# Performance work log

Measured on AMD Instinct MI355X. Metric: run time of the kernel, lower is better.

The kernel has to match this reference:

```python
import jax, jax.numpy as jnp
import numpy as np

N = 50000   # nodes
E = 800000  # edges
F = 256     # in_channels
H = 256     # hidden (GCN output)


def setup_inputs() -> dict:
    key = jax.random.key(0)
    ks = jax.random.split(key, 6)
    x = jax.random.normal(ks[0], (N, F), jnp.float32)
    edge_index = jax.random.randint(ks[1], (2, E), 0, N)
    perm = jax.random.permutation(ks[2], N)
    W = jax.random.normal(ks[3], (F, H), jnp.float32) / np.sqrt(F)
    b = jnp.zeros((H,), jnp.float32)
    a = jnp.full((1,), 0.25, jnp.float32)  # PReLU slope
    disc_W = jax.random.normal(ks[4], (H, H), jnp.float32) / np.sqrt(H)
    return {"x": x, "W": W, "b": b, "a": a, "disc_W": disc_W,
            "edge_index": edge_index, "perm": perm}


def _gcn(x, W, b, src, dst, n):
    # GCNConv: linear -> symmetric-normalized aggregation (with self-loops) -> bias
    xw = x @ W  # [N, H]
    loop = jnp.arange(n)
    s = jnp.concatenate([src, loop])
    d = jnp.concatenate([dst, loop])
    ew = jnp.ones(s.shape[0], xw.dtype)
    deg = jax.ops.segment_sum(ew, d, num_segments=n)          # [N]
    dinv = jnp.where(deg > 0, jax.lax.rsqrt(deg), 0.0)
    norm = dinv[s] * dinv[d]                                   # [E+N]
    out = jax.ops.segment_sum(xw[s] * norm[:, None], d, num_segments=n)
    return out + b


def reference(x, W, b, a, disc_W, edge_index, perm):
    src, dst = edge_index[0], edge_index[1]
    n = x.shape[0]

    def encode(feat):
        h = _gcn(feat, W, b, src, dst, n)
        return jnp.where(h >= 0, h, a * h)  # PReLU

    z1 = encode(x)          # clean
    z2 = encode(x[perm])    # corrupted (row permutation)
    summary = jax.nn.sigmoid(z1.mean(axis=0))  # [H]
    wsum = disc_W @ summary                     # [H]
    pos = z1 @ wsum  # [N]
    neg = z2 @ wsum  # [N]
    return pos, neg
```

## Files before the change

kernel.cpp:

```cpp
#include <hip/hip_runtime.h>

#define N_NODES 50000
#define N_EDGES 800000
#define DIM 256
#define NB 196
#define UNROLL 8
#define MAXE (N_EDGES + N_NODES * UNROLL)
#define CSB 128
#define NCH 4
#define CCOLS 64
#define CHSZ (N_NODES * CCOLS)
#define RPB 16
#define CHB (N_NODES / RPB)

typedef __attribute__((ext_vector_type(8))) short bf16x8;
typedef __attribute__((ext_vector_type(4))) float f32x4;
typedef __attribute__((ext_vector_type(2))) float f32x2;

__device__ __forceinline__ unsigned int f2bf(float f) {
  unsigned int u = __float_as_uint(f);
  return (u + 0x7FFFu + ((u >> 16) & 1u)) >> 16;
}
__device__ __forceinline__ float bf_lo(unsigned int u) {
  return __uint_as_float(u << 16);
}
__device__ __forceinline__ float bf_hi(unsigned int u) {
  return __uint_as_float(u & 0xFFFF0000u);
}


__global__ void k_deg(const int* __restrict__ dst, int* __restrict__ deg) {
  int e = blockIdx.x * blockDim.x + threadIdx.x;
  if (e < N_EDGES) atomicAdd(&deg[dst[e]], 1);
}

__global__ __launch_bounds__(256) void k_alloc(const int* __restrict__ deg,
                                               float* __restrict__ dinv,
                                               int* __restrict__ gcur,
                                               int2* __restrict__ rse,
                                               int* __restrict__ cursor,
                                               uint2* __restrict__ meta) {
  __shared__ int s[256];
  __shared__ int base;
  const int t = threadIdx.x;
  const int i = blockIdx.x * 256 + t;
  int d = 0, pd = 0;
  if (i < N_NODES) {
    d = deg[i];
    dinv[i] = rsqrtf((float)(d + 1));
    pd = (d + UNROLL - 1) & ~(UNROLL - 1);
  }
  s[t] = pd;
  __syncthreads();
  for (int off = 1; off < 256; off <<= 1) {
    int u = (t >= off) ? s[t - off] : 0;
    __syncthreads();
    s[t] += u;
    __syncthreads();
  }
  if (t == 255) base = atomicAdd(gcur, s[255]);
  __syncthreads();
  if (i < N_NODES) {
    int rs = base + s[t] - pd;
    rse[i] = make_int2(rs, rs + pd);
    cursor[i] = rs;
    for (int j = d; j < pd; ++j) meta[rs + j] = make_uint2(0u, 0u);
  }
}

__global__ void k_scatter(const int* __restrict__ src, const int* __restrict__ dst,
                          const int* __restrict__ perm, const float* __restrict__ dinv,
                          int* __restrict__ cursor, uint2* __restrict__ meta) {
  int e = blockIdx.x * blockDim.x + threadIdx.x;
  if (e < N_EDGES) {
    int s = src[e], d = dst[e];
    int p = atomicAdd(&cursor[d], 1);
    meta[p] = make_uint2((unsigned)s | ((unsigned)perm[s] << 16),
                         __float_as_uint(dinv[s] * dinv[d]));
  }
}


__global__ void k_prep(const float* __restrict__ W, ushort* __restrict__ Wt) {
  int n = blockIdx.x, k = threadIdx.x;
  Wt[n * DIM + k] = (ushort)f2bf(W[k * DIM + n]);
}


__global__ __launch_bounds__(256) void k_gemm(const float* __restrict__ X,
                                              const ushort* __restrict__ Wt,
                                              ushort* __restrict__ XWC) {
  __shared__ ushort Xs[64 * 40];
  __shared__ ushort Ws[256 * 40];
  const int tid = threadIdx.x;
  const int lane = tid & 63;
  const int w = tid >> 6;
  const int m0 = blockIdx.x * 64;
  const int l16 = lane & 15, kh = lane >> 4;

  f32x4 acc[4][4];
#pragma unroll
  for (int mf = 0; mf < 4; ++mf)
#pragma unroll
    for (int nf = 0; nf < 4; ++nf) acc[mf][nf] = (f32x4){0.f, 0.f, 0.f, 0.f};

  for (int k0 = 0; k0 < DIM; k0 += 32) {
#pragma unroll
    for (int it = 0; it < 2; ++it) {
      int idx = tid + it * 256;
      int row = idx >> 3, q = idx & 7;
      int grow = m0 + row;
      float4 v = make_float4(0.f, 0.f, 0.f, 0.f);
      if (grow < N_NODES)
        v = *reinterpret_cast<const float4*>(&X[(size_t)grow * DIM + k0 + q * 4]);
      uint2 p;
      p.x = f2bf(v.x) | (f2bf(v.y) << 16);
      p.y = f2bf(v.z) | (f2bf(v.w) << 16);
      *reinterpret_cast<uint2*>(&Xs[row * 40 + q * 4]) = p;
    }
#pragma unroll
    for (int it = 0; it < 4; ++it) {
      int idx = tid + it * 256;
      int n = idx >> 2, c = idx & 3;
      uint4 wv = *reinterpret_cast<const uint4*>(&Wt[n * DIM + k0 + c * 8]);
      *reinterpret_cast<uint4*>(&Ws[n * 40 + c * 8]) = wv;
    }
    __syncthreads();
    bf16x8 a[4], b[4];
#pragma unroll
    for (int f = 0; f < 4; ++f) {
      a[f] = *reinterpret_cast<const bf16x8*>(&Ws[(w * 64 + f * 16 + l16) * 40 + kh * 8]);
      b[f] = *reinterpret_cast<const bf16x8*>(&Xs[(f * 16 + l16) * 40 + kh * 8]);
    }
#pragma unroll
    for (int mf = 0; mf < 4; ++mf)
#pragma unroll
      for (int nf = 0; nf < 4; ++nf)
        acc[mf][nf] = __builtin_amdgcn_mfma_f32_16x16x32_bf16(a[nf], b[mf],
                                                              acc[mf][nf], 0, 0, 0);
    __syncthreads();
  }
#pragma unroll
  for (int mf = 0; mf < 4; ++mf) {
    int m = m0 + mf * 16 + l16;
    if (m >= N_NODES) continue;
#pragma unroll
    for (int nf = 0; nf < 4; ++nf) {
      int cb = nf * 16 + kh * 4;
      uint2 p;
      p.x = f2bf(acc[mf][nf][0]) | (f2bf(acc[mf][nf][1]) << 16);
      p.y = f2bf(acc[mf][nf][2]) | (f2bf(acc[mf][nf][3]) << 16);
      *reinterpret_cast<uint2*>(&XWC[(size_t)w * CHSZ + (size_t)m * CCOLS + cb]) = p;
    }
  }
}


__device__ __forceinline__ void fma8v(f32x2* A, uint4 v, f32x2 n) {
  A[0] += (f32x2){__uint_as_float(v.x << 16), __uint_as_float(v.x)} * n;
  A[1] += (f32x2){__uint_as_float(v.y << 16), __uint_as_float(v.y)} * n;
  A[2] += (f32x2){__uint_as_float(v.z << 16), __uint_as_float(v.z)} * n;
  A[3] += (f32x2){__uint_as_float(v.w << 16), __uint_as_float(v.w)} * n;
}

__global__ __launch_bounds__(256) void k_aggc(
    const ushort* __restrict__ xwc, const int2* __restrict__ rse,
    const uint2* __restrict__ meta, const int* __restrict__ perm,
    const float* __restrict__ dinv, const float* __restrict__ bias,
    const float* __restrict__ slope, ushort* __restrict__ z1,
    ushort* __restrict__ z2) {
  const int blk = blockIdx.x;
  const int ch = blk / CHB;
  const int rb = blk % CHB;
  const int tid = threadIdx.x;
  const int r = rb * RPB + (tid >> 4);
  const int l = tid & 15;
  const int eg = l >> 3;
  const int sc = l & 7;
  const ushort* xc = xwc + (size_t)ch * CHSZ;
  const ushort* xcs = xc + sc * 8;
  const uint2* mp = meta + eg * 2;

  f32x2 a1[4] = {{0.f, 0.f}, {0.f, 0.f}, {0.f, 0.f}, {0.f, 0.f}};
  f32x2 a2[4] = {{0.f, 0.f}, {0.f, 0.f}, {0.f, 0.f}, {0.f, 0.f}};
  const int2 se = rse[r];
  int e = se.x;
  const int eEnd = se.y;
  if (e < eEnd) {
    uint4 m0 = *reinterpret_cast<const uint4*>(mp + e);
    uint4 m1 = *reinterpret_cast<const uint4*>(mp + e + 4);
    while (e < eEnd) {
      uint4 vA1 = *reinterpret_cast<const uint4*>(xcs + ((m0.x & 0xFFFFu) << 6));
      uint4 vA2 = *reinterpret_cast<const uint4*>(xcs + ((m0.x >> 16) << 6));
      uint4 vB1 = *reinterpret_cast<const uint4*>(xcs + ((m0.z & 0xFFFFu) << 6));
      uint4 vB2 = *reinterpret_cast<const uint4*>(xcs + ((m0.z >> 16) << 6));
      uint4 vC1 = *reinterpret_cast<const uint4*>(xcs + ((m1.x & 0xFFFFu) << 6));
      uint4 vC2 = *reinterpret_cast<const uint4*>(xcs + ((m1.x >> 16) << 6));
      uint4 vD1 = *reinterpret_cast<const uint4*>(xcs + ((m1.z & 0xFFFFu) << 6));
      uint4 vD2 = *reinterpret_cast<const uint4*>(xcs + ((m1.z >> 16) << 6));
      const int en = e + 8;
      const int ep = (en < eEnd) ? en : e;
      uint4 m0n = *reinterpret_cast<const uint4*>(mp + ep);
      uint4 m1n = *reinterpret_cast<const uint4*>(mp + ep + 4);
      const float fA = __uint_as_float(m0.y), fB = __uint_as_float(m0.w);
      const float fC = __uint_as_float(m1.y), fD = __uint_as_float(m1.w);
      const f32x2 nA = {fA, fA}, nB = {fB, fB}, nC = {fC, fC}, nD = {fD, fD};
      fma8v(a1, vA1, nA); fma8v(a2, vA2, nA);
      fma8v(a1, vB1, nB); fma8v(a2, vB2, nB);
      fma8v(a1, vC1, nC); fma8v(a2, vC2, nC);
      fma8v(a1, vD1, nD); fma8v(a2, vD2, nD);
      m0 = m0n; m1 = m1n;
      e = en;
    }
  }
#pragma unroll
  for (int j = 0; j < 4; ++j) {
    a1[j].x += __shfl_xor(a1[j].x, 8);
    a1[j].y += __shfl_xor(a1[j].y, 8);
    a2[j].x += __shfl_xor(a2[j].x, 8);
    a2[j].y += __shfl_xor(a2[j].y, 8);
  }
  if (eg == 0) {
    const float di = dinv[r];
    const float d2 = di * di;
    const f32x2 nd = {d2, d2};
    const int pr = perm[r];
    uint4 s1 = *reinterpret_cast<const uint4*>(xcs + ((unsigned)r << 6));
    uint4 s2 = *reinterpret_cast<const uint4*>(xcs + ((unsigned)pr << 6));
    fma8v(a1, s1, nd); fma8v(a2, s2, nd);
    const float* bp = bias + ch * CCOLS + sc * 8;
    float4 b0 = *reinterpret_cast<const float4*>(bp);
    float4 b1 = *reinterpret_cast<const float4*>(bp + 4);
    a1[0] += (f32x2){b0.x, b0.y}; a1[1] += (f32x2){b0.z, b0.w};
    a1[2] += (f32x2){b1.x, b1.y}; a1[3] += (f32x2){b1.z, b1.w};
    a2[0] += (f32x2){b0.x, b0.y}; a2[1] += (f32x2){b0.z, b0.w};
    a2[2] += (f32x2){b1.x, b1.y}; a2[3] += (f32x2){b1.z, b1.w};
    const float a0 = slope[0];
#pragma unroll
    for (int j = 0; j < 4; ++j) {
      a1[j].x = a1[j].x >= 0.f ? a1[j].x : a0 * a1[j].x;
      a1[j].y = a1[j].y >= 0.f ? a1[j].y : a0 * a1[j].y;
      a2[j].x = a2[j].x >= 0.f ? a2[j].x : a0 * a2[j].x;
      a2[j].y = a2[j].y >= 0.f ? a2[j].y : a0 * a2[j].y;
    }
    uint4 p1, p2;
    p1.x = f2bf(a1[0].x) | (f2bf(a1[0].y) << 16);
    p1.y = f2bf(a1[1].x) | (f2bf(a1[1].y) << 16);
    p1.z = f2bf(a1[2].x) | (f2bf(a1[2].y) << 16);
    p1.w = f2bf(a1[3].x) | (f2bf(a1[3].y) << 16);
    p2.x = f2bf(a2[0].x) | (f2bf(a2[0].y) << 16);
    p2.y = f2bf(a2[1].x) | (f2bf(a2[1].y) << 16);
    p2.z = f2bf(a2[2].x) | (f2bf(a2[2].y) << 16);
    p2.w = f2bf(a2[3].x) | (f2bf(a2[3].y) << 16);
    const size_t o = (size_t)r * DIM + ch * CCOLS + sc * 8;
    *reinterpret_cast<uint4*>(z1 + o) = p1;
    *reinterpret_cast<uint4*>(z2 + o) = p2;
  }
}


__global__ __launch_bounds__(256) void k_colsum(const ushort* __restrict__ z1,
                                                float* __restrict__ partial) {
  __shared__ float red[8 * 256];
  const int t = threadIdx.x;
  const int c8 = t & 31;
  const int g = t >> 5;
  float s[8] = {0.f, 0.f, 0.f, 0.f, 0.f, 0.f, 0.f, 0.f};
  for (int r = blockIdx.x * 8 + g; r < N_NODES; r += 8 * CSB) {
    uint4 v = *reinterpret_cast<const uint4*>(z1 + (size_t)r * DIM + c8 * 8);
    s[0] += bf_lo(v.x); s[1] += bf_hi(v.x);
    s[2] += bf_lo(v.y); s[3] += bf_hi(v.y);
    s[4] += bf_lo(v.z); s[5] += bf_hi(v.z);
    s[6] += bf_lo(v.w); s[7] += bf_hi(v.w);
  }
#pragma unroll
  for (int j = 0; j < 8; ++j) red[g * 256 + c8 * 8 + j] = s[j];
  __syncthreads();
  float tot = 0.f;
#pragma unroll
  for (int g2 = 0; g2 < 8; ++g2) tot += red[g2 * 256 + t];
  partial[blockIdx.x * 256 + t] = tot;
}

__global__ __launch_bounds__(256) void k_wsum(const float* __restrict__ partial,
                                              const float* __restrict__ disc_W,
                                              float* __restrict__ wsum) {
  __shared__ float s[DIM];
  const int t = threadIdx.x;
  float a0 = 0.f, a1 = 0.f, a2 = 0.f, a3 = 0.f;
  for (int b = 0; b < CSB; b += 4) {
    a0 += partial[(b + 0) * 256 + t];
    a1 += partial[(b + 1) * 256 + t];
    a2 += partial[(b + 2) * 256 + t];
    a3 += partial[(b + 3) * 256 + t];
  }
  float m = (a0 + a1 + a2 + a3) * (1.0f / (float)N_NODES);
  s[t] = 1.0f / (1.0f + expf(-m));
  __syncthreads();
  float acc = 0.f;
  for (int j = 0; j < DIM; j += 4) {
    float4 w4 = *reinterpret_cast<const float4*>(&disc_W[t * DIM + j]);
    acc += w4.x * s[j] + w4.y * s[j + 1] + w4.z * s[j + 2] + w4.w * s[j + 3];
  }
  wsum[t] = acc;
}


__global__ __launch_bounds__(256) void k_posneg(const ushort* __restrict__ z1,
                                                const ushort* __restrict__ z2,
                                                const float* __restrict__ wsum,
                                                float* __restrict__ pos,
                                                float* __restrict__ neg) {
  const int wid = (blockIdx.x * blockDim.x + threadIdx.x) >> 6;
  const int lane = threadIdx.x & 63;
  if (wid >= N_NODES) return;
  uint2 v1 = *reinterpret_cast<const uint2*>(z1 + (size_t)wid * DIM + lane * 4);
  uint2 v2 = *reinterpret_cast<const uint2*>(z2 + (size_t)wid * DIM + lane * 4);
  float4 w4 = *reinterpret_cast<const float4*>(&wsum[lane * 4]);
  float dp = bf_lo(v1.x) * w4.x + bf_hi(v1.x) * w4.y + bf_lo(v1.y) * w4.z + bf_hi(v1.y) * w4.w;
  float dn = bf_lo(v2.x) * w4.x + bf_hi(v2.x) * w4.y + bf_lo(v2.y) * w4.z + bf_hi(v2.y) * w4.w;
#pragma unroll
  for (int off = 32; off > 0; off >>= 1) {
    dp += __shfl_down(dp, off);
    dn += __shfl_down(dn, off);
  }
  if (lane == 0) { pos[wid] = dp; neg[wid] = dn; }
}


extern "C" void kernel_launch(void* const* d_in, const int* in_sizes, int n_in,
                              void* d_out, int out_size, void* d_ws, size_t ws_size,
                              hipStream_t stream) {
  const float* x      = (const float*)d_in[0];
  const float* W      = (const float*)d_in[1];
  const float* b      = (const float*)d_in[2];
  const float* a      = (const float*)d_in[3];
  const float* disc_W = (const float*)d_in[4];
  const int*   eidx   = (const int*)d_in[5];
  const int*   perm   = (const int*)d_in[6];
  const int* src = eidx;
  const int* dst = eidx + N_EDGES;

  constexpr size_t SZ_BFM  = (size_t)N_NODES * DIM * 2;
  constexpr size_t SZ_META = (size_t)MAXE * 8;
  constexpr size_t OFF_XWC = 0;
  constexpr size_t OFF_Z1  = OFF_XWC + SZ_BFM;
  constexpr size_t OFF_Z2  = OFF_Z1 + SZ_BFM;
  constexpr size_t OFF_WT  = OFF_Z2 + SZ_BFM;
  constexpr size_t OFF_DEG = OFF_WT + 131072;
  constexpr size_t OFF_GC  = OFF_DEG + 200000;
  constexpr size_t OFF_DNV = OFF_DEG + 200192;
  constexpr size_t OFF_RSE = OFF_DNV + 200192;
  constexpr size_t OFF_CUR = OFF_RSE + 400128;
  constexpr size_t OFF_MT  = OFF_CUR + 200192;
  constexpr size_t OFF_WSM = OFF_MT + SZ_META;
  constexpr size_t OFF_PT  = OFF_WSM + 1024;
  constexpr size_t NEED    = OFF_PT + (size_t)CSB * 256 * 4;
  if (ws_size < NEED) return;

  char* ws = (char*)d_ws;
  ushort* xwc    = (ushort*)(ws + OFF_XWC);
  ushort* z1     = (ushort*)(ws + OFF_Z1);
  ushort* z2     = (ushort*)(ws + OFF_Z2);
  ushort* Wt     = (ushort*)(ws + OFF_WT);
  int*    deg    = (int*)(ws + OFF_DEG);
  int*    gcur   = (int*)(ws + OFF_GC);
  float*  dinv   = (float*)(ws + OFF_DNV);
  int2*   rse    = (int2*)(ws + OFF_RSE);
  int*    cursor = (int*)(ws + OFF_CUR);
  uint2*  meta   = (uint2*)(ws + OFF_MT);
  float*  wsum   = (float*)(ws + OFF_WSM);
  float*  partial= (float*)(ws + OFF_PT);

  float* pos = (float*)d_out;
  float* neg = pos + N_NODES;

  hipMemsetAsync(deg, 0, 200192, stream);

  k_deg<<<(N_EDGES + 255) / 256, 256, 0, stream>>>(dst, deg);
  k_alloc<<<NB, 256, 0, stream>>>(deg, dinv, gcur, rse, cursor, meta);
  k_scatter<<<(N_EDGES + 255) / 256, 256, 0, stream>>>(src, dst, perm, dinv,
                                                       cursor, meta);

  k_prep<<<DIM, DIM, 0, stream>>>(W, Wt);
  k_gemm<<<(N_NODES + 63) / 64, 256, 0, stream>>>(x, Wt, xwc);

  k_aggc<<<NCH * CHB, 256, 0, stream>>>(xwc, rse, meta, perm, dinv, b, a, z1, z2);

  k_colsum<<<CSB, 256, 0, stream>>>(z1, partial);
  k_wsum<<<1, 256, 0, stream>>>(partial, disc_W, wsum);
  k_posneg<<<(N_NODES * 64 + 255) / 256, 256, 0, stream>>>(z1, z2, wsum, pos, neg);
}
```

Before: 244.9 us.

## Enlarge GEMM tile to 128 rows and fuse wsum into colsum via last-block

```diff
diff --git a/kernel.cpp b/kernel.cpp
--- a/kernel.cpp
+++ b/kernel.cpp
@@ -87,15 +87,16 @@
 }
 
 
-__global__ __launch_bounds__(256) void k_gemm(const float* __restrict__ X,
+__global__ __launch_bounds__(512) void k_gemm(const float* __restrict__ X,
                                               const ushort* __restrict__ Wt,
                                               ushort* __restrict__ XWC) {
-  __shared__ ushort Xs[64 * 40];
+  __shared__ ushort Xs[128 * 40];
   __shared__ ushort Ws[256 * 40];
   const int tid = threadIdx.x;
   const int lane = tid & 63;
   const int w = tid >> 6;
-  const int m0 = blockIdx.x * 64;
+  const int wm = w >> 2, wn = w & 3;
+  const int m0 = blockIdx.x * 128;
   const int l16 = lane & 15, kh = lane >> 4;
 
   f32x4 acc[4][4];
@@ -107,7 +108,7 @@
   for (int k0 = 0; k0 < DIM; k0 += 32) {
 #pragma unroll
     for (int it = 0; it < 2; ++it) {
-      int idx = tid + it * 256;
+      int idx = tid + it * 512;
       int row = idx >> 3, q = idx & 7;
       int grow = m0 + row;
       float4 v = make_float4(0.f, 0.f, 0.f, 0.f);
@@ -119,8 +120,8 @@
       *reinterpret_cast<uint2*>(&Xs[row * 40 + q * 4]) = p;
     }
 #pragma unroll
-    for (int it = 0; it < 4; ++it) {
-      int idx = tid + it * 256;
+    for (int it = 0; it < 2; ++it) {
+      int idx = tid + it * 512;
       int n = idx >> 2, c = idx & 3;
       uint4 wv = *reinterpret_cast<const uint4*>(&Wt[n * DIM + k0 + c * 8]);
       *reinterpret_cast<uint4*>(&Ws[n * 40 + c * 8]) = wv;
@@ -129,8 +130,8 @@
     bf16x8 a[4], b[4];
 #pragma unroll
     for (int f = 0; f < 4; ++f) {
-      a[f] = *reinterpret_cast<const bf16x8*>(&Ws[(w * 64 + f * 16 + l16) * 40 + kh * 8]);
-      b[f] = *reinterpret_cast<const bf16x8*>(&Xs[(f * 16 + l16) * 40 + kh * 8]);
+      a[f] = *reinterpret_cast<const bf16x8*>(&Ws[(wn * 64 + f * 16 + l16) * 40 + kh * 8]);
+      b[f] = *reinterpret_cast<const bf16x8*>(&Xs[(wm * 64 + f * 16 + l16) * 40 + kh * 8]);
     }
 #pragma unroll
     for (int mf = 0; mf < 4; ++mf)
@@ -142,15 +143,16 @@
   }
 #pragma unroll
   for (int mf = 0; mf < 4; ++mf) {
-    int m = m0 + mf * 16 + l16;
+    int m = m0 + wm * 64 + mf * 16 + l16;
     if (m >= N_NODES) continue;
 #pragma unroll
     for (int nf = 0; nf < 4; ++nf) {
-      int cb = nf * 16 + kh * 4;
+      int nb = wn * 64 + nf * 16 + kh * 4;
       uint2 p;
       p.x = f2bf(acc[mf][nf][0]) | (f2bf(acc[mf][nf][1]) << 16);
       p.y = f2bf(acc[mf][nf][2]) | (f2bf(acc[mf][nf][3]) << 16);
-      *reinterpret_cast<uint2*>(&XWC[(size_t)w * CHSZ + (size_t)m * CCOLS + cb]) = p;
+      *reinterpret_cast<uint2*>(
+          &XWC[(size_t)(nb >> 6) * CHSZ + (size_t)m * CCOLS + (nb & 63)]) = p;
     }
   }
 }
@@ -260,7 +262,10 @@
 
 
 __global__ __launch_bounds__(256) void k_colsum(const ushort* __restrict__ z1,
-                                                float* __restrict__ partial) {
+                                                const float* __restrict__ disc_W,
+                                                float* __restrict__ partial,
+                                                float* __restrict__ wsum,
+                                                int* __restrict__ done) {
   __shared__ float red[8 * 256];
   const int t = threadIdx.x;
   const int c8 = t & 31;
@@ -280,13 +285,12 @@
 #pragma unroll
   for (int g2 = 0; g2 < 8; ++g2) tot += red[g2 * 256 + t];
   partial[blockIdx.x * 256 + t] = tot;
-}
-
-__global__ __launch_bounds__(256) void k_wsum(const float* __restrict__ partial,
-                                              const float* __restrict__ disc_W,
-                                              float* __restrict__ wsum) {
-  __shared__ float s[DIM];
-  const int t = threadIdx.x;
+  __threadfence();
+  __shared__ int lastflag;
+  if (t == 0) lastflag = (atomicAdd(done, 1) == CSB - 1) ? 1 : 0;
+  __syncthreads();
+  if (!lastflag) return;
+  __shared__ float sm[DIM];
   float a0 = 0.f, a1 = 0.f, a2 = 0.f, a3 = 0.f;
   for (int b = 0; b < CSB; b += 4) {
     a0 += partial[(b + 0) * 256 + t];
@@ -295,12 +299,12 @@
     a3 += partial[(b + 3) * 256 + t];
   }
   float m = (a0 + a1 + a2 + a3) * (1.0f / (float)N_NODES);
-  s[t] = 1.0f / (1.0f + expf(-m));
+  sm[t] = 1.0f / (1.0f + expf(-m));
   __syncthreads();
   float acc = 0.f;
   for (int j = 0; j < DIM; j += 4) {
     float4 w4 = *reinterpret_cast<const float4*>(&disc_W[t * DIM + j]);
-    acc += w4.x * s[j] + w4.y * s[j + 1] + w4.z * s[j + 2] + w4.w * s[j + 3];
+    acc += w4.x * sm[j] + w4.y * sm[j + 1] + w4.z * sm[j + 2] + w4.w * sm[j + 3];
   }
   wsum[t] = acc;
 }
@@ -349,6 +353,7 @@
   constexpr size_t OFF_WT  = OFF_Z2 + SZ_BFM;
   constexpr size_t OFF_DEG = OFF_WT + 131072;
   constexpr size_t OFF_GC  = OFF_DEG + 200000;
+  constexpr size_t OFF_DONE= OFF_GC + 4;
   constexpr size_t OFF_DNV = OFF_DEG + 200192;
   constexpr size_t OFF_RSE = OFF_DNV + 200192;
   constexpr size_t OFF_CUR = OFF_RSE + 400128;
@@ -365,6 +370,7 @@
   ushort* Wt     = (ushort*)(ws + OFF_WT);
   int*    deg    = (int*)(ws + OFF_DEG);
   int*    gcur   = (int*)(ws + OFF_GC);
+  int*    done   = (int*)(ws + OFF_DONE);
   float*  dinv   = (float*)(ws + OFF_DNV);
   int2*   rse    = (int2*)(ws + OFF_RSE);
   int*    cursor = (int*)(ws + OFF_CUR);
@@ -383,11 +389,10 @@
                                                        cursor, meta);
 
   k_prep<<<DIM, DIM, 0, stream>>>(W, Wt);
-  k_gemm<<<(N_NODES + 63) / 64, 256, 0, stream>>>(x, Wt, xwc);
+  k_gemm<<<(N_NODES + 127) / 128, 512, 0, stream>>>(x, Wt, xwc);
 
   k_aggc<<<NCH * CHB, 256, 0, stream>>>(xwc, rse, meta, perm, dinv, b, a, z1, z2);
 
-  k_colsum<<<CSB, 256, 0, stream>>>(z1, partial);
-  k_wsum<<<1, 256, 0, stream>>>(partial, disc_W, wsum);
+  k_colsum<<<CSB, 256, 0, stream>>>(z1, disc_W, partial, wsum, done);
   k_posneg<<<(N_NODES * 64 + 255) / 256, 256, 0, stream>>>(z1, z2, wsum, pos, neg);
 }
```

New measurement: 247.9 us. No clear change (+1.2%).
